# Performance work log

Hardware: AMD Instinct MI355X
Metric: run time of the kernel (lower is better)

## Reference

```python
import jax, jax.numpy as jnp
import numpy as np

B, T, D, P, NP = 32, 512, 512, 200, 8
RADIUS = 3
TEMP = 1.0
DIRECTION = 'right'
NEG = -100000.0
EPS_NORM = 1e-12


def setup_inputs() -> dict:
    key = jax.random.key(0)
    k1, k2, k3 = jax.random.split(key, 3)
    return {
        "x": jax.random.normal(k1, (B, T, D), dtype=jnp.float32),
        "timeline_mask": jnp.ones((B, T), dtype=jnp.float32),
        "prototype_vectors": jax.random.uniform(k2, (P, D, NP), dtype=jnp.float32),
        "patch_select": jax.random.normal(k3, (1, P, NP), dtype=jnp.float32),
    }


def _l2norm(v, axis):
    return v / jnp.maximum(jnp.linalg.norm(v, axis=axis, keepdims=True), EPS_NORM)


def reference(x, timeline_mask, prototype_vectors, patch_select):
    # --- subpatch_dist ---
    xn = _l2norm(x, axis=-1)                       # (B, T, D)
    pn = _l2norm(prototype_vectors, axis=1)        # (P, D, n_p)
    dist_all = jnp.einsum('btd,pdi->bpti', xn, pn)  # (B, P, T, n_p)

    # timeline mask
    tm = timeline_mask[:, None, :, None]
    dist_all = dist_all * tm + (1.0 - tm) * NEG

    dt = dist_all.dtype
    b, p, t, n_p = dist_all.shape
    ar_t = jnp.arange(t)

    mask_act = jnp.ones((b, p, t), dt)
    mask_subpatch = jnp.ones((b, p, n_p), dt)
    mask_all = jnp.ones((b, p, t, n_p), dt)
    adjacent = jnp.ones((b, p, t), dt)

    ids_list, vals_list, ev_list = [], [], []
    # greedy iterative max-select over the n_p subpatches (sequential dependency)
    for it in range(n_p):
        dm = dist_all + (1.0 - mask_all * adjacent[..., None]) * NEG
        max_subs = dm.max(axis=2)                   # (B, P, n_p) best score per subpatch
        max_subs_id = jnp.argmax(dm, axis=2)        # (B, P, n_p) best event per subpatch
        max_sub_act = max_subs.max(axis=-1)         # (B, P)
        sub_id = jnp.argmax(max_subs, axis=-1)      # (B, P) chosen subpatch
        event_id = jnp.take_along_axis(max_subs_id, sub_id[..., None], axis=2)[..., 0]  # (B, P)

        neigh = (jnp.abs(ar_t[None, None, :] - event_id[..., None]) <= RADIUS).astype(dt)
        if it > 0:
            if DIRECTION == 'right':
                dmask = (ar_t[None, None, :] > event_id[..., None]).astype(dt)
            else:
                dmask = (ar_t[None, None, :] < event_id[..., None]).astype(dt)
            neigh = neigh * dmask
        adjacent = neigh

        # suppress chosen event and chosen subpatch (scatter_ 0 == multiply by 1-onehot)
        mask_act = mask_act * (1.0 - jax.nn.one_hot(event_id, t, dtype=dt))
        mask_subpatch = mask_subpatch * (1.0 - jax.nn.one_hot(sub_id, n_p, dtype=dt))
        mask_all = mask_all * mask_act[..., None] * mask_subpatch[:, :, None, :]

        ids_list.append(sub_id)
        vals_list.append(max_sub_act)
        ev_list.append(event_id.astype(dt))

    subpatch_ids = jnp.stack(ids_list, axis=-1)   # (B, P, n_p) int
    values = jnp.stack(vals_list, axis=-1)        # (B, P, n_p)
    indices = jnp.stack(ev_list, axis=-1)         # (B, P, n_p) float, matches torch cat promotion

    order = jnp.argsort(subpatch_ids, axis=-1)    # unique ids -> deterministic permutation
    values_r = jnp.take_along_axis(values, order, axis=-1)
    indices_r = jnp.take_along_axis(indices, order, axis=-1)

    slots = jax.nn.sigmoid(patch_select * TEMP)           # (1, P, n_p)
    factor = slots.sum(-1, keepdims=True) + 1e-10
    values_slot = values_r * (slots * n_p / factor)
    max_activation_slots = values_slot.sum(-1)            # (B, P)
    min_distances = n_p - max_activation_slots
    return (max_activation_slots, min_distances, indices_r)
```

## Files before the change

### kernel.cpp

```cpp
#include <hip/hip_runtime.h>
#include <hip/hip_bf16.h>
#include <hip/hip_fp16.h>
#include <math.h>

#define B_    32
#define T_    512
#define D_    512
#define P_    200
#define NP_   8
#define N_TOT 1600
#define NEG_  (-100000.0f)
#define LO_SCALE 2048.0f
#define LO_INV   (1.0f/2048.0f)

typedef __attribute__((ext_vector_type(8))) _Float16 f16x8;
typedef __attribute__((ext_vector_type(4))) _Float16 f16x4;
typedef __attribute__((ext_vector_type(4))) float   f32x4;

#define GLL16(gp, lp) __builtin_amdgcn_global_load_lds( \
    (const __attribute__((address_space(1))) void*)(gp), \
    (__attribute__((address_space(3))) void*)(lp), 16, 0, 0)

__device__ __forceinline__ float wave_reduce_sum(float v) {
#pragma unroll
  for (int off = 32; off; off >>= 1) v += __shfl_xor(v, off, 64);
  return v;
}

__global__ __launch_bounds__(256) void norm_x_kernel(const float* __restrict__ x,
                                                     _Float16* __restrict__ xh,
                                                     _Float16* __restrict__ xl) {
  int row  = blockIdx.x * 4 + (threadIdx.x >> 6);
  int lane = threadIdx.x & 63;
  const float* xr = x + (size_t)row * D_;
  float4 v0 = *(const float4*)(xr + lane * 4);
  float4 v1 = *(const float4*)(xr + 256 + lane * 4);
  float s = v0.x*v0.x + v0.y*v0.y + v0.z*v0.z + v0.w*v0.w
          + v1.x*v1.x + v1.y*v1.y + v1.z*v1.z + v1.w*v1.w;
  s = wave_reduce_sum(s);
  float dn = fmaxf(sqrtf(s), 1e-12f);
  float f[8] = {v0.x/dn, v0.y/dn, v0.z/dn, v0.w/dn, v1.x/dn, v1.y/dn, v1.z/dn, v1.w/dn};
  f16x4 h0, h1, l0, l1;
#pragma unroll
  for (int j = 0; j < 4; j++) {
    h0[j] = (_Float16)f[j];
    l0[j] = (_Float16)((f[j] - (float)h0[j]) * LO_SCALE);
    h1[j] = (_Float16)f[4 + j];
    l1[j] = (_Float16)((f[4 + j] - (float)h1[j]) * LO_SCALE);
  }
  size_t base = (size_t)row * D_;
  *(f16x4*)(xh + base + lane * 4)       = h0;
  *(f16x4*)(xh + base + 256 + lane * 4) = h1;
  *(f16x4*)(xl + base + lane * 4)       = l0;
  *(f16x4*)(xl + base + 256 + lane * 4) = l1;
}

__global__ __launch_bounds__(256) void norm_w_kernel(const float* __restrict__ proto,
                                                     _Float16* __restrict__ wh,
                                                     _Float16* __restrict__ wl) {
  int n    = blockIdx.x * 4 + (threadIdx.x >> 6);
  int lane = threadIdx.x & 63;
  int p = n >> 3, i = n & 7;
  float v[8];
  float s = 0.f;
#pragma unroll
  for (int k = 0; k < 8; k++) {
    int d = k * 64 + lane;
    v[k] = proto[((size_t)p * D_ + d) * NP_ + i];
    s += v[k] * v[k];
  }
  s = wave_reduce_sum(s);
  float dn = fmaxf(sqrtf(s), 1e-12f);
  size_t base = (size_t)n * D_;
#pragma unroll
  for (int k = 0; k < 8; k++) {
    float f = v[k] / dn;
    _Float16 h = (_Float16)f;
    wh[base + k * 64 + lane] = h;
    wl[base + k * 64 + lane] = (_Float16)((f - (float)h) * LO_SCALE);
  }
}

__global__ __launch_bounds__(256, 2) void gemm_mfma(
    const _Float16* __restrict__ XH, const _Float16* __restrict__ XL,
    const _Float16* __restrict__ WH, const _Float16* __restrict__ WL,
    const float* __restrict__ tm, float* __restrict__ dist) {
  __shared__ _Float16 lds[2 * 16384];
  const int b  = blockIdx.z;
  const int n0 = blockIdx.y * 128;
  const int t0 = blockIdx.x * 128;
  const int tid = threadIdx.x;
  const int w = tid >> 6, l = tid & 63;
  const int fr = l & 15;
  const int lk = (l >> 4) * 8;

  const _Float16* pHi[4]; const _Float16* pLo[4];
  int dstoff;
  {
    int H = w >> 1;
    if ((w & 1) == 0) {
#pragma unroll
      for (int m = 0; m < 4; m++) {
        int row = n0 + H * 64 + m * 16 + fr;
        if (row > N_TOT - 1) row = N_TOT - 1;
        pHi[m] = WH + (size_t)row * D_ + lk;
        pLo[m] = WL + (size_t)row * D_ + lk;
      }
      dstoff = H * 2048;
    } else {
#pragma unroll
      for (int m = 0; m < 4; m++) {
        int col = t0 + H * 64 + m * 16 + fr;
        pHi[m] = XH + ((size_t)b * T_ + col) * D_ + lk;
        pLo[m] = XL + ((size_t)b * T_ + col) * D_ + lk;
      }
      dstoff = 8192 + H * 2048;
    }
  }

#define STAGE(bufoff, kk) do { \
    _Float16* dh = &lds[(bufoff) + dstoff]; \
    _Float16* dl = dh + 4096; \
    GLL16(pHi[0] + (kk), dh);        GLL16(pHi[1] + (kk), dh + 512); \
    GLL16(pHi[2] + (kk), dh + 1024); GLL16(pHi[3] + (kk), dh + 1536); \
    GLL16(pLo[0] + (kk), dl);        GLL16(pLo[1] + (kk), dl + 512); \
    GLL16(pLo[2] + (kk), dl + 1024); GLL16(pLo[3] + (kk), dl + 1536); \
  } while (0)

  const int aB = (w >> 1) * 2048;
  const int xB = 8192 + (w & 1) * 2048;

  f32x4 acch[4][4], accc[4][4];
#pragma unroll
  for (int m = 0; m < 4; m++)
#pragma unroll
    for (int n = 0; n < 4; n++) { acch[m][n] = (f32x4)0.0f; accc[m][n] = (f32x4)0.0f; }

  STAGE(0, 0);
  __syncthreads();

  for (int kt = 0; kt < 16; ++kt) {
    const int cur = (kt & 1) * 16384;
    if (kt < 15) STAGE(cur ^ 16384, (kt + 1) * 32);

    f16x8 ah[4], al[4], bh[4], bl[4];
#pragma unroll
    for (int m = 0; m < 4; m++) {
      ah[m] = *(const f16x8*)&lds[cur + aB + m * 512 + l * 8];
      al[m] = *(const f16x8*)&lds[cur + aB + 4096 + m * 512 + l * 8];
    }
#pragma unroll
    for (int n = 0; n < 4; n++) {
      bh[n] = *(const f16x8*)&lds[cur + xB + n * 512 + l * 8];
      bl[n] = *(const f16x8*)&lds[cur + xB + 4096 + n * 512 + l * 8];
    }
#pragma unroll
    for (int m = 0; m < 4; m++)
#pragma unroll
      for (int n = 0; n < 4; n++) {
        acch[m][n] = __builtin_amdgcn_mfma_f32_16x16x32_f16(ah[m], bh[n], acch[m][n], 0, 0, 0);
        accc[m][n] = __builtin_amdgcn_mfma_f32_16x16x32_f16(ah[m], bl[n], accc[m][n], 0, 0, 0);
        accc[m][n] = __builtin_amdgcn_mfma_f32_16x16x32_f16(al[m], bh[n], accc[m][n], 0, 0, 0);
      }
    __syncthreads();
  }

  const int fq = l >> 4;
#pragma unroll
  for (int n = 0; n < 4; n++) {
    int col = t0 + (w & 1) * 64 + n * 16 + fr;
    float tmc = tm[b * T_ + col];
#pragma unroll
    for (int m = 0; m < 4; m++) {
      int nb = n0 + (w >> 1) * 64 + m * 16 + fq * 4;
#pragma unroll
      for (int r = 0; r < 4; r++) {
        int nr = nb + r;
        if (nr < N_TOT) {
          float v = acch[m][n][r] + accc[m][n][r] * LO_INV;
          v = v * tmc + (1.0f - tmc) * NEG_;
          dist[((size_t)b * N_TOT + nr) * T_ + col] = v;
        }
      }
    }
  }
#undef STAGE
}

__global__ __launch_bounds__(256) void select_kernel(const float* __restrict__ dist,
                                                     const float* __restrict__ tmg,
                                                     const float* __restrict__ psel,
                                                     float* __restrict__ out) {
  int w = threadIdx.x >> 6, lane = threadIdx.x & 63;
  int pair = blockIdx.x * 4 + w;
  int b = pair / P_, p = pair % P_;
  const float* dbase = dist + ((size_t)b * N_TOT + p * NP_) * T_;

  bool okt = true;
#pragma unroll
  for (int c = 0; c < 8; c++) okt = okt && (tmg[b * T_ + c * 64 + lane] == 1.0f);
  bool tmones = (__ballot(okt) == ~0ULL);

  float rv = -3.0e38f; int rkey = 0x7FFFFFFF;
  float qv = -3.0e38f; int qkey = 0x7FFFFFFF;
#pragma unroll
  for (int i = 0; i < 8; i++) {
    const float* row = dbase + (size_t)i * T_;
    float4 u0 = *(const float4*)(row + lane * 8);
    float4 u1 = *(const float4*)(row + lane * 8 + 4);
    float uv[8] = {u0.x, u0.y, u0.z, u0.w, u1.x, u1.y, u1.z, u1.w};
#pragma unroll
    for (int j = 0; j < 8; j++) {
      int key = i * T_ + lane * 8 + j;
      float v = uv[j];
      if (v > rv) { rv = v; rkey = key; }
      float q = v + NEG_;
      if (q > qv) { qv = q; qkey = key; }
    }
  }
#pragma unroll
  for (int off = 32; off; off >>= 1) {
    float ov = __shfl_xor(rv, off, 64); int okk = __shfl_xor(rkey, off, 64);
    if (ov > rv || (ov == rv && okk < rkey)) { rv = ov; rkey = okk; }
    float o2 = __shfl_xor(qv, off, 64); int ok2 = __shfl_xor(qkey, off, 64);
    if (o2 > qv || (o2 == qv && ok2 < qkey)) { qv = o2; qkey = ok2; }
  }

  float valh[8]; int evh[8], sidh[8];
#pragma unroll
  for (int k = 0; k < 8; k++) { valh[k] = 0.f; evh[k] = -1; sidh[k] = 0; }
  unsigned msub = 0xFFu;
  int e_last = 0;

  for (int it = 0; it < 8; ++it) {
    float bv; int bkey;
    if (tmones) {
      if (it == 0) { bv = rv; bkey = rkey; }
      else {
        int i = lane >> 3, widx = lane & 7;
        int tw, nw;
        if (it == 1) { tw = e_last - 3 + widx; nw = 7; }
        else         { tw = e_last + 1 + widx; nw = 3; }
        bool valid = (widx < nw) && (tw >= 0) && (tw < T_) && (((msub >> i) & 1u) != 0u);
#pragma unroll
        for (int k = 0; k < 8; k++) if (tw == evh[k]) valid = false;
        float v  = valid ? dbase[(size_t)i * T_ + tw] : -3.0e38f;
        int  key = valid ? (i * T_ + tw) : 0x7FFFFFFF;
#pragma unroll
        for (int off = 32; off; off >>= 1) {
          float ov = __shfl_xor(v, off, 64);
          int  ok2 = __shfl_xor(key, off, 64);
          if (ov > v || (ov == v && ok2 < key)) { v = ov; key = ok2; }
        }
        if (v > -2.9e38f) { bv = v; bkey = key; }
        else              { bv = qv; bkey = qkey; }
      }
    } else {
      float lv = -3.0e38f; int lkey = 0x7FFFFFFF;
      for (int i = 0; i < 8; i++) {
        bool sub_ok = ((msub >> i) & 1u) != 0u;
        const float* row = dbase + (size_t)i * T_;
        float4 u0 = *(const float4*)(row + lane * 8);
        float4 u1 = *(const float4*)(row + lane * 8 + 4);
        float uv[8] = {u0.x, u0.y, u0.z, u0.w, u1.x, u1.y, u1.z, u1.w};
#pragma unroll
        for (int j = 0; j < 8; j++) {
          int t = lane * 8 + j;
          bool act = sub_ok;
          if (it > 0) {
            int dt = t - e_last;
            act = act && (dt <= 3) && (dt >= -3);
            if (it > 1) act = act && (dt > 0);
          }
#pragma unroll
          for (int k = 0; k < 8; k++) if (t == evh[k]) act = false;
          float dm = act ? uv[j] : (uv[j] + NEG_);
          if (dm > lv) { lv = dm; lkey = i * T_ + t; }
        }
      }
#pragma unroll
      for (int off = 32; off; off >>= 1) {
        float ov = __shfl_xor(lv, off, 64);
        int  ok2 = __shfl_xor(lkey, off, 64);
        if (ov > lv || (ov == lv && ok2 < lkey)) { lv = ov; lkey = ok2; }
      }
      bv = lv; bkey = lkey;
    }
    int bi = bkey >> 9, bt = bkey & (T_ - 1);
#pragma unroll
    for (int k = 0; k < 8; k++) {
      if (it == k) { valh[k] = bv; evh[k] = bt; sidh[k] = bi; }
    }
    msub &= ~(1u << bi);
    e_last = bt;
  }

  if (lane == 0) {
    int ord[8]; unsigned used = 0;
#pragma unroll
    for (int j = 0; j < 8; j++) {
      int bk = 1 << 30, bi2 = 0;
#pragma unroll
      for (int k = 0; k < 8; k++)
        if (!((used >> k) & 1u)) { int key = sidh[k] * 8 + k; if (key < bk) { bk = key; bi2 = k; } }
      ord[j] = bi2; used |= 1u << bi2;
    }
    float slots[8]; float ssum = 0.f;
#pragma unroll
    for (int i = 0; i < 8; i++) {
      slots[i] = 1.0f / (1.0f + expf(-psel[p * NP_ + i]));
      ssum += slots[i];
    }
    float fac = ssum + 1e-10f;
    float acc = 0.f;
    float vr[8]; float er[8];
#pragma unroll
    for (int j = 0; j < 8; j++) {
      float vv = 0.f, ee = 0.f;
#pragma unroll
      for (int k = 0; k < 8; k++) if (ord[j] == k) { vv = valh[k]; ee = (float)evh[k]; }
      vr[j] = vv; er[j] = ee;
    }
#pragma unroll
    for (int j = 0; j < 8; j++) acc += vr[j] * (slots[j] * 8.0f / fac);
    int bp = b * P_ + p;
    out[bp] = acc;
    out[B_ * P_ + bp] = 8.0f - acc;
#pragma unroll
    for (int j = 0; j < 8; j++) out[2 * B_ * P_ + bp * 8 + j] = er[j];
  }
}

extern "C" void kernel_launch(void* const* d_in, const int* in_sizes, int n_in,
                              void* d_out, int out_size, void* d_ws, size_t ws_size,
                              hipStream_t stream) {
  const float* x     = (const float*)d_in[0];
  const float* tm    = (const float*)d_in[1];
  const float* proto = (const float*)d_in[2];
  const float* psel  = (const float*)d_in[3];
  float* out = (float*)d_out;

  char* wsb = (char*)d_ws;
  _Float16* XH = (_Float16*)wsb;
  _Float16* XL = (_Float16*)(wsb + 16777216u);
  _Float16* WH = (_Float16*)(wsb + 2u * 16777216u);
  _Float16* WL = (_Float16*)(wsb + 2u * 16777216u + 1638400u);
  float*   dist = (float*)(wsb + 2u * 16777216u + 2u * 1638400u);

  norm_x_kernel<<<dim3(B_ * T_ / 4), 256, 0, stream>>>(x, XH, XL);
  norm_w_kernel<<<dim3(N_TOT / 4), 256, 0, stream>>>(proto, WH, WL);
  gemm_mfma<<<dim3(T_ / 128, (N_TOT + 127) / 128, B_), 256, 0, stream>>>(XH, XL, WH, WL, tm, dist);
  select_kernel<<<dim3(B_ * P_ / 4), 256, 0, stream>>>(dist, tm, psel, out);
}
```

Baseline: 260.2 us.

## Fuse per-prototype argmax into GEMM epilogue via packed atomicMax slots

```diff
diff --git a/kernel.cpp b/kernel.cpp
--- a/kernel.cpp
+++ b/kernel.cpp
@@ -16,6 +16,7 @@
 typedef __attribute__((ext_vector_type(8))) _Float16 f16x8;
 typedef __attribute__((ext_vector_type(4))) _Float16 f16x4;
 typedef __attribute__((ext_vector_type(4))) float   f32x4;
+typedef unsigned long long u64;
 
 #define GLL16(gp, lp) __builtin_amdgcn_global_load_lds( \
     (const __attribute__((address_space(1))) void*)(gp), \
@@ -25,6 +26,23 @@
 #pragma unroll
   for (int off = 32; off; off >>= 1) v += __shfl_xor(v, off, 64);
   return v;
+}
+
+__device__ __forceinline__ unsigned ordf(float f) {
+  unsigned u = __float_as_uint(f);
+  return (u & 0x80000000u) ? ~u : (u | 0x80000000u);
+}
+__device__ __forceinline__ float deco(unsigned o) {
+  unsigned u = (o & 0x80000000u) ? (o ^ 0x80000000u) : ~o;
+  return __uint_as_float(u);
+}
+__device__ __forceinline__ u64 packvk(float v, int key) {
+  return ((u64)ordf(v) << 32) | (u64)(4095 - key);
+}
+
+__global__ void init_slots(u64* s) {
+  int i = blockIdx.x * 256 + threadIdx.x;
+  if (i < 2 * B_ * P_) s[i] = 0ULL;
 }
 
 __global__ __launch_bounds__(256) void norm_x_kernel(const float* __restrict__ x,
@@ -81,11 +99,12 @@
   }
 }
 
-__global__ __launch_bounds__(256, 2) void gemm_mfma(
+__global__ __launch_bounds__(256, 4) void gemm_mfma(
     const _Float16* __restrict__ XH, const _Float16* __restrict__ XL,
     const _Float16* __restrict__ WH, const _Float16* __restrict__ WL,
-    const float* __restrict__ tm, float* __restrict__ dist) {
-  __shared__ _Float16 lds[2 * 16384];
+    const float* __restrict__ tm, float* __restrict__ dist,
+    u64* __restrict__ rawslot, u64* __restrict__ qslot) {
+  __shared__ _Float16 lds[16384];
   const int b  = blockIdx.z;
   const int n0 = blockIdx.y * 128;
   const int t0 = blockIdx.x * 128;
@@ -118,8 +137,8 @@
     }
   }
 
-#define STAGE(bufoff, kk) do { \
-    _Float16* dh = &lds[(bufoff) + dstoff]; \
+#define STAGE(kk) do { \
+    _Float16* dh = &lds[dstoff]; \
     _Float16* dl = dh + 4096; \
     GLL16(pHi[0] + (kk), dh);        GLL16(pHi[1] + (kk), dh + 512); \
     GLL16(pHi[2] + (kk), dh + 1024); GLL16(pHi[3] + (kk), dh + 1536); \
@@ -136,23 +155,19 @@
 #pragma unroll
     for (int n = 0; n < 4; n++) { acch[m][n] = (f32x4)0.0f; accc[m][n] = (f32x4)0.0f; }
 
-  STAGE(0, 0);
-  __syncthreads();
-
   for (int kt = 0; kt < 16; ++kt) {
-    const int cur = (kt & 1) * 16384;
-    if (kt < 15) STAGE(cur ^ 16384, (kt + 1) * 32);
-
+    STAGE(kt * 32);
+    __syncthreads();
     f16x8 ah[4], al[4], bh[4], bl[4];
 #pragma unroll
     for (int m = 0; m < 4; m++) {
-      ah[m] = *(const f16x8*)&lds[cur + aB + m * 512 + l * 8];
-      al[m] = *(const f16x8*)&lds[cur + aB + 4096 + m * 512 + l * 8];
+      ah[m] = *(const f16x8*)&lds[aB + m * 512 + l * 8];
+      al[m] = *(const f16x8*)&lds[aB + 4096 + m * 512 + l * 8];
     }
 #pragma unroll
     for (int n = 0; n < 4; n++) {
-      bh[n] = *(const f16x8*)&lds[cur + xB + n * 512 + l * 8];
-      bl[n] = *(const f16x8*)&lds[cur + xB + 4096 + n * 512 + l * 8];
+      bh[n] = *(const f16x8*)&lds[xB + n * 512 + l * 8];
+      bl[n] = *(const f16x8*)&lds[xB + 4096 + n * 512 + l * 8];
     }
 #pragma unroll
     for (int m = 0; m < 4; m++)
@@ -166,6 +181,9 @@
   }
 
   const int fq = l >> 4;
+  u64 pm[4], qm[4];
+#pragma unroll
+  for (int m = 0; m < 4; m++) { pm[m] = 0ULL; qm[m] = 0ULL; }
 #pragma unroll
   for (int n = 0; n < 4; n++) {
     int col = t0 + (w & 1) * 64 + n * 16 + fr;
@@ -180,14 +198,40 @@
           float v = acch[m][n][r] + accc[m][n][r] * LO_INV;
           v = v * tmc + (1.0f - tmc) * NEG_;
           dist[((size_t)b * N_TOT + nr) * T_ + col] = v;
+          int key = ((fq * 4 + r) & 7) * T_ + col;
+          u64 pk = packvk(v, key);
+          if (pk > pm[m]) pm[m] = pk;
+          u64 qk = packvk(v + NEG_, key);
+          if (qk > qm[m]) qm[m] = qk;
         }
       }
     }
   }
+#pragma unroll
+  for (int m = 0; m < 4; m++) {
+#pragma unroll
+    for (int off = 1; off <= 16; off <<= 1) {
+      u64 o1 = __shfl_xor(pm[m], off, 64); if (o1 > pm[m]) pm[m] = o1;
+      u64 o2 = __shfl_xor(qm[m], off, 64); if (o2 > qm[m]) qm[m] = o2;
+    }
+  }
+  if ((l & 31) == 0) {
+    int h = l >> 5;
+#pragma unroll
+    for (int m = 0; m < 4; m++) {
+      int p = (n0 >> 3) + ((w >> 1) * 8) + m * 2 + h;
+      if (p < P_) {
+        atomicMax(&rawslot[b * P_ + p], pm[m]);
+        atomicMax(&qslot[b * P_ + p], qm[m]);
+      }
+    }
+  }
 #undef STAGE
 }
 
 __global__ __launch_bounds__(256) void select_kernel(const float* __restrict__ dist,
+                                                     const u64* __restrict__ rawslot,
+                                                     const u64* __restrict__ qslot,
                                                      const float* __restrict__ tmg,
                                                      const float* __restrict__ psel,
                                                      float* __restrict__ out) {
@@ -201,30 +245,9 @@
   for (int c = 0; c < 8; c++) okt = okt && (tmg[b * T_ + c * 64 + lane] == 1.0f);
   bool tmones = (__ballot(okt) == ~0ULL);
 
-  float rv = -3.0e38f; int rkey = 0x7FFFFFFF;
-  float qv = -3.0e38f; int qkey = 0x7FFFFFFF;
-#pragma unroll
-  for (int i = 0; i < 8; i++) {
-    const float* row = dbase + (size_t)i * T_;
-    float4 u0 = *(const float4*)(row + lane * 8);
-    float4 u1 = *(const float4*)(row + lane * 8 + 4);
-    float uv[8] = {u0.x, u0.y, u0.z, u0.w, u1.x, u1.y, u1.z, u1.w};
-#pragma unroll
-    for (int j = 0; j < 8; j++) {
-      int key = i * T_ + lane * 8 + j;
-      float v = uv[j];
-      if (v > rv) { rv = v; rkey = key; }
-      float q = v + NEG_;
-      if (q > qv) { qv = q; qkey = key; }
-    }
-  }
-#pragma unroll
-  for (int off = 32; off; off >>= 1) {
-    float ov = __shfl_xor(rv, off, 64); int okk = __shfl_xor(rkey, off, 64);
-    if (ov > rv || (ov == rv && okk < rkey)) { rv = ov; rkey = okk; }
-    float o2 = __shfl_xor(qv, off, 64); int ok2 = __shfl_xor(qkey, off, 64);
-    if (o2 > qv || (o2 == qv && ok2 < qkey)) { qv = o2; qkey = ok2; }
-  }
+  u64 rs = rawslot[pair], qs = qslot[pair];
+  float rv = deco((unsigned)(rs >> 32)); int rkey = 4095 - (int)(rs & 0xFFFFu);
+  float qv = deco((unsigned)(qs >> 32)); int qkey = 4095 - (int)(qs & 0xFFFFu);
 
   float valh[8]; int evh[8], sidh[8];
 #pragma unroll
@@ -346,9 +369,13 @@
   _Float16* WH = (_Float16*)(wsb + 2u * 16777216u);
   _Float16* WL = (_Float16*)(wsb + 2u * 16777216u + 1638400u);
   float*   dist = (float*)(wsb + 2u * 16777216u + 2u * 1638400u);
-
+  u64*  rawslot = (u64*)(wsb + 141688832u);
+  u64*  qslot   = rawslot + B_ * P_;
+
+  init_slots<<<dim3(50), 256, 0, stream>>>(rawslot);
   norm_x_kernel<<<dim3(B_ * T_ / 4), 256, 0, stream>>>(x, XH, XL);
   norm_w_kernel<<<dim3(N_TOT / 4), 256, 0, stream>>>(proto, WH, WL);
-  gemm_mfma<<<dim3(T_ / 128, (N_TOT + 127) / 128, B_), 256, 0, stream>>>(XH, XL, WH, WL, tm, dist);
-  select_kernel<<<dim3(B_ * P_ / 4), 256, 0, stream>>>(dist, tm, psel, out);
-}
+  gemm_mfma<<<dim3(T_ / 128, (N_TOT + 127) / 128, B_), 256, 0, stream>>>(
+      XH, XL, WH, WL, tm, dist, rawslot, qslot);
+  select_kernel<<<dim3(B_ * P_ / 4), 256, 0, stream>>>(dist, rawslot, qslot, tm, psel, out);
+}
```

Measured after the change: 747.1 us. +187.1%, slower.
